# Optimization experiments

Measured on AMD Instinct MI355X. Metric: run time of the kernel, lower is better.

## Reference

```python
import jax, jax.numpy as jnp
import numpy as np

B, D, N_CLASSES = 8192, 128, 50


def setup_inputs() -> dict:
    key = jax.random.key(0)
    k1, k2, k3 = jax.random.split(key, 3)
    anchor = jax.random.normal(k1, (B, D), dtype=jnp.float32)
    target = jax.random.normal(k2, (B, D), dtype=jnp.float32)
    labels = jax.random.randint(k3, (B,), 0, N_CLASSES)
    return {"anchor": anchor, "target": target, "labels": labels}


def reference(anchor, target, labels):
    # Faithful vectorization of QuadrupletLoss.nt_xent_loss.
    # Note: the original hardcodes temperature 0.05 (ignores self.temp).
    TEMP = 0.05
    n = labels.shape[0]
    diff = labels[:, None] != labels[None, :]                      # mask2: [B,B]
    same_off = (labels[:, None] == labels[None, :]) & ~jnp.eye(n, dtype=bool)  # mask

    # d[j, m] = <anchor[j], target[m]> / 0.05
    d = jnp.matmul(anchor, target.T) / TEMP                        # [B,B]
    neg = jnp.where(diff, d, -jnp.inf)
    mx = jax.lax.stop_gradient(jnp.max(neg, axis=1))               # maxdot.detach() per j
    mx = jnp.where(jnp.isfinite(mx), mx, 0.0)
    # s[j] = sum_{m: labels[m]!=labels[j]} exp(d[j,m] - mx[j])  (exp(-inf)=0 masks out)
    s = jnp.sum(jnp.exp(neg - mx[:, None]), axis=1)                # [B]

    # Inner double loop: nds[i] = sum over j with labels[j]!=labels[i] of s[j]
    difff = diff.astype(s.dtype)
    nds = difff @ s                                                # [B]
    negcount = jnp.sum(difff, axis=1)                              # negtivesum

    x = jnp.where(negcount > 0, nds / jnp.where(negcount > 0, negcount, 1.0), nds)
    log_prob = -jnp.log(x + 1e-12)                                 # constant across cols
    mask_sum = jnp.sum(same_off, axis=1)
    # (mask * log_prob).sum(1) / clamp(mask_sum,1) == log_prob where mask_sum>0 else 0
    pos_logits = jnp.where(mask_sum > 0, log_prob, 0.0)
    return -jnp.mean(pos_logits)
```

## Files before the change

### kernel.cpp

```cpp
#include <hip/hip_runtime.h>
#include <float.h>
#include <math.h>

typedef __attribute__((ext_vector_type(8))) short short8;
typedef __attribute__((ext_vector_type(8))) _Float16 half8;
typedef __attribute__((ext_vector_type(4))) float f32x4;

constexpr int B_N  = 8192;
constexpr int D_KK = 128;
constexpr int NCLS = 50;
constexpr int NCHUNK = 8;
constexpr int BLK_ROWS = 64;
constexpr int TCOLS = 64;
constexpr float C_SCALE = 28.853900817779268f;
constexpr float MARGIN  = 40.0f;
constexpr float NEG_LOW  = -1.0e5f;
constexpr float NEG_MASK = -1.0e30f;

__device__ __forceinline__ float exp2fast(float x) { return __builtin_amdgcn_exp2f(x); }

__device__ __forceinline__ void async_copy16(void* lds, const void* g) {
    __builtin_amdgcn_global_load_lds((const __attribute__((address_space(1))) unsigned int*)g,
                                     (__attribute__((address_space(3))) unsigned int*)lds,
                                     16, 0, 0);
}

__global__ void tof16_kernel(const float* __restrict__ a, const float* __restrict__ b,
                             short* __restrict__ aH, short* __restrict__ bH)
{
    const int NPER = B_N * D_KK / 8;
    int i = blockIdx.x * blockDim.x + threadIdx.x;
    const float* src = (i < NPER) ? a : b;
    short*       dst = (i < NPER) ? aH : bH;
    const float  sc  = (i < NPER) ? C_SCALE : 1.0f;
    int j = (i < NPER) ? i : i - NPER;
    const f32x4* sp = (const f32x4*)(src + (size_t)j * 8);
    f32x4 v0 = sp[0], v1 = sp[1];
    short8 h;
#pragma unroll
    for (int e = 0; e < 4; ++e) {
        h[e]     = __builtin_bit_cast(short, (_Float16)(sc * v0[e]));
        h[e + 4] = __builtin_bit_cast(short, (_Float16)(sc * v1[e]));
    }
    *(short8*)(dst + (size_t)j * 8) = h;
}

__global__ __launch_bounds__(256, 4)
void rowstats_kernel(const short* __restrict__ aH, const short* __restrict__ bH,
                     const int* __restrict__ labels,
                     float* __restrict__ pmx, float* __restrict__ ps)
{
    __shared__ __align__(16) char bbuf[2][TCOLS * 256];
    __shared__ float mergebuf[BLK_ROWS][2];

    const int bid   = blockIdx.x;
    const int chunk = bid & (NCHUNK - 1);
    const int R0 = (bid >> 3) * BLK_ROWS;
    const int C0 = chunk * (B_N / NCHUNK);

    const int tid = threadIdx.x;
    const int wid = tid >> 6, l = tid & 63;
    const int l15 = l & 15, l16 = l >> 4;
    const int wr = wid >> 1, wc = wid & 1;

    half8 aF[2][4];
#pragma unroll
    for (int mf = 0; mf < 2; ++mf) {
        const int arow = R0 + wr * 32 + mf * 16 + l15;
#pragma unroll
        for (int ks = 0; ks < 4; ++ks)
            aF[mf][ks] = __builtin_bit_cast(half8,
                *(const short8*)(aH + (size_t)arow * D_KK + ks * 32 + l16 * 8));
    }

    int labA[8];
#pragma unroll
    for (int mf = 0; mf < 2; ++mf)
#pragma unroll
        for (int r = 0; r < 4; ++r)
            labA[mf * 4 + r] = labels[R0 + wr * 32 + mf * 16 + l16 * 4 + r];

    float mx[8], sm[8];
#pragma unroll
    for (int i = 0; i < 8; ++i) { mx[i] = NEG_LOW; sm[i] = 0.0f; }

    const int NT = (B_N / NCHUNK) / TCOLS;

#define STAGE(tile, bsel)                                                            \
    {                                                                                \
        _Pragma("unroll")                                                            \
        for (int q = 0; q < 4; ++q) {                                                \
            int col = q * 16 + (tid >> 4);                                           \
            int gslot = (tid & 15) ^ (col & 7);                                      \
            const short* gp = bH + (size_t)(C0 + (tile) * TCOLS + col) * D_KK + gslot * 8; \
            char* lp = &bbuf[bsel][q * 4096 + tid * 16];                             \
            async_copy16(lp, gp);                                                    \
        }                                                                            \
    }

    STAGE(0, 0);
    __syncthreads();

    for (int t = 0; t < NT; ++t) {
        const int cur = t & 1;
        if (t + 1 < NT) STAGE(t + 1, cur ^ 1);

        f32x4 acc[2][2];
#pragma unroll
        for (int mf = 0; mf < 2; ++mf)
#pragma unroll
            for (int nf = 0; nf < 2; ++nf) acc[mf][nf] = f32x4{0.f, 0.f, 0.f, 0.f};

#pragma unroll
        for (int ks = 0; ks < 4; ++ks) {
            half8 bF[2];
#pragma unroll
            for (int nf = 0; nf < 2; ++nf) {
                int col  = wc * 32 + nf * 16 + l15;
                int slot = (ks * 4 + l16) ^ (col & 7);
                bF[nf] = __builtin_bit_cast(half8,
                    *(const short8*)(&bbuf[cur][col * 256 + slot * 16]));
            }
#pragma unroll
            for (int mf = 0; mf < 2; ++mf)
#pragma unroll
                for (int nf = 0; nf < 2; ++nf)
                    acc[mf][nf] = __builtin_amdgcn_mfma_f32_16x16x32_f16(
                        aF[mf][ks], bF[nf], acc[mf][nf], 0, 0, 0);
        }

        const int colB = C0 + t * TCOLS;
        int lB[2];
#pragma unroll
        for (int nf = 0; nf < 2; ++nf) lB[nf] = labels[colB + wc * 32 + nf * 16 + l15];

#pragma unroll
        for (int mf = 0; mf < 2; ++mf) {
            float gm = fmaxf(fmaxf(fmaxf(acc[mf][0][0], acc[mf][0][1]),
                                   fmaxf(acc[mf][0][2], acc[mf][0][3])),
                             fmaxf(fmaxf(acc[mf][1][0], acc[mf][1][1]),
                                   fmaxf(acc[mf][1][2], acc[mf][1][3])));
            int sk = 1;
#pragma unroll
            for (int r = 0; r < 4; ++r) sk &= (gm < mx[mf * 4 + r] - MARGIN) ? 1 : 0;
            if (!__all(sk)) {
#pragma unroll
                for (int r = 0; r < 4; ++r) {
                    const int i = mf * 4 + r;
                    float v0 = (lB[0] != labA[i]) ? acc[mf][0][r] : NEG_MASK;
                    float v1 = (lB[1] != labA[i]) ? acc[mf][1][r] : NEG_MASK;
                    float nm = fmaxf(mx[i], fmaxf(v0, v1));
                    float e  = exp2fast(v0 - nm) + exp2fast(v1 - nm);
                    sm[i] = sm[i] * exp2fast(mx[i] - nm) + e;
                    mx[i] = nm;
                }
            }
        }
        __syncthreads();
    }

#pragma unroll
    for (int i = 0; i < 8; ++i) {
#pragma unroll
        for (int off = 1; off < 16; off <<= 1) {
            float m2 = __shfl_xor(mx[i], off);
            float s2 = __shfl_xor(sm[i], off);
            float nm = fmaxf(mx[i], m2);
            sm[i] = sm[i] * exp2fast(mx[i] - nm) + s2 * exp2fast(m2 - nm);
            mx[i] = nm;
        }
    }

    if (wc == 1 && l15 == 0) {
#pragma unroll
        for (int mf = 0; mf < 2; ++mf)
#pragma unroll
            for (int r = 0; r < 4; ++r) {
                int rl = wr * 32 + mf * 16 + l16 * 4 + r;
                mergebuf[rl][0] = mx[mf * 4 + r];
                mergebuf[rl][1] = sm[mf * 4 + r];
            }
    }
    __syncthreads();
    if (wc == 0 && l15 == 0) {
#pragma unroll
        for (int mf = 0; mf < 2; ++mf)
#pragma unroll
            for (int r = 0; r < 4; ++r) {
                const int i = mf * 4 + r;
                int rl = wr * 32 + mf * 16 + l16 * 4 + r;
                float m2 = mergebuf[rl][0], s2 = mergebuf[rl][1];
                float nm = fmaxf(mx[i], m2);
                float s  = sm[i] * exp2fast(mx[i] - nm) + s2 * exp2fast(m2 - nm);
                pmx[chunk * B_N + R0 + rl] = nm;
                ps [chunk * B_N + R0 + rl] = s;
            }
    }
#undef STAGE
}

__global__ void classsum_kernel(const float* __restrict__ pmx, const float* __restrict__ ps,
                                const int* __restrict__ labels,
                                float* __restrict__ classSum, unsigned int* __restrict__ classCnt)
{
    __shared__ float        csL[NCLS];
    __shared__ unsigned int ccL[NCLS];
    int t = threadIdx.x;
    if (t < NCLS) { csL[t] = 0.0f; ccL[t] = 0u; }
    __syncthreads();

    int j = blockIdx.x * blockDim.x + t;
    float m = -FLT_MAX, s = 0.0f;
#pragma unroll
    for (int c = 0; c < NCHUNK; ++c) {
        float m2 = pmx[(size_t)c * B_N + j];
        float s2 = ps [(size_t)c * B_N + j];
        float nm = fmaxf(m, m2);
        s = s * exp2fast(m - nm) + s2 * exp2fast(m2 - nm);
        m = nm;
    }
    int lab = labels[j];
    atomicAdd(&csL[lab], s);
    atomicAdd(&ccL[lab], 1u);
    __syncthreads();
    if (t < NCLS) {
        atomicAdd(&classSum[t], csL[t]);
        atomicAdd(&classCnt[t], ccL[t]);
    }
}

__global__ void loss_kernel(const float* __restrict__ classSum,
                            const unsigned int* __restrict__ classCnt,
                            float* __restrict__ out)
{
    int c = threadIdx.x;
    float cs        = (c < NCLS) ? classSum[c] : 0.0f;
    unsigned int cc = (c < NCLS) ? classCnt[c] : 0u;

    float tot = cs;
#pragma unroll
    for (int off = 1; off < 64; off <<= 1) tot += __shfl_xor(tot, off);

    float contrib = 0.0f;
    if (c < NCLS && cc > 0u) {
        float negc = (float)(B_N - (int)cc);
        float nds  = tot - cs;
        float x    = (negc > 0.0f) ? (nds / negc) : nds;
        float lp   = (cc >= 2u) ? (-logf(x + 1e-12f)) : 0.0f;
        contrib = (float)cc * lp;
    }
#pragma unroll
    for (int off = 1; off < 64; off <<= 1) contrib += __shfl_xor(contrib, off);
    if (c == 0) out[0] = -(contrib / (float)B_N);
}

extern "C" void kernel_launch(void* const* d_in, const int* in_sizes, int n_in,
                              void* d_out, int out_size, void* d_ws, size_t ws_size,
                              hipStream_t stream)
{
    const float* anchor = (const float*)d_in[0];
    const float* target = (const float*)d_in[1];
    const int*   labels = (const int*)d_in[2];
    float* out = (float*)d_out;

    const size_t PLANE = (size_t)B_N * D_KK * sizeof(short);
    char* ws = (char*)d_ws;
    short* aH = (short*)(ws + 0 * PLANE);
    short* bH = (short*)(ws + 1 * PLANE);
    float* ps  = (float*)(ws + 2 * PLANE);
    float* pmx = (float*)(ws + 2 * PLANE + sizeof(float) * NCHUNK * B_N);
    char*  cls = ws + 2 * PLANE + 2 * sizeof(float) * NCHUNK * B_N;
    float*        classSum = (float*)cls;
    unsigned int* classCnt = (unsigned int*)(cls + 256);

    hipMemsetAsync(classSum, 0, 512, stream);

    tof16_kernel<<<2 * (B_N * D_KK / 8) / 256, 256, 0, stream>>>(anchor, target, aH, bH);
    rowstats_kernel<<<(B_N / BLK_ROWS) * NCHUNK, 256, 0, stream>>>(aH, bH, labels, pmx, ps);
    classsum_kernel<<<B_N / 256, 256, 0, stream>>>(pmx, ps, labels, classSum, classCnt);
    loss_kernel<<<1, 64, 0, stream>>>(classSum, classCnt, out);
}
```

Before: 57.36 us.

## Drop LDS staging; load B fragments directly from global in k-major layout

```diff
diff --git a/kernel.cpp b/kernel.cpp
--- a/kernel.cpp
+++ b/kernel.cpp
@@ -9,9 +9,8 @@
 constexpr int B_N  = 8192;
 constexpr int D_KK = 128;
 constexpr int NCLS = 50;
-constexpr int NCHUNK = 8;
-constexpr int BLK_ROWS = 64;
-constexpr int TCOLS = 64;
+constexpr int NCHUNK = 16;
+constexpr int CCOLS = B_N / NCHUNK;
 constexpr float C_SCALE = 28.853900817779268f;
 constexpr float MARGIN  = 40.0f;
 constexpr float NEG_LOW  = -1.0e5f;
@@ -19,54 +18,56 @@
 
 __device__ __forceinline__ float exp2fast(float x) { return __builtin_amdgcn_exp2f(x); }
 
-__device__ __forceinline__ void async_copy16(void* lds, const void* g) {
-    __builtin_amdgcn_global_load_lds((const __attribute__((address_space(1))) unsigned int*)g,
-                                     (__attribute__((address_space(3))) unsigned int*)lds,
-                                     16, 0, 0);
-}
-
-__global__ void tof16_kernel(const float* __restrict__ a, const float* __restrict__ b,
-                             short* __restrict__ aH, short* __restrict__ bH)
+__global__ void prep_kernel(const float* __restrict__ a, const float* __restrict__ b,
+                            short* __restrict__ aH, short* __restrict__ bT)
 {
     const int NPER = B_N * D_KK / 8;
     int i = blockIdx.x * blockDim.x + threadIdx.x;
-    const float* src = (i < NPER) ? a : b;
-    short*       dst = (i < NPER) ? aH : bH;
-    const float  sc  = (i < NPER) ? C_SCALE : 1.0f;
-    int j = (i < NPER) ? i : i - NPER;
-    const f32x4* sp = (const f32x4*)(src + (size_t)j * 8);
-    f32x4 v0 = sp[0], v1 = sp[1];
-    short8 h;
-#pragma unroll
-    for (int e = 0; e < 4; ++e) {
-        h[e]     = __builtin_bit_cast(short, (_Float16)(sc * v0[e]));
-        h[e + 4] = __builtin_bit_cast(short, (_Float16)(sc * v1[e]));
-    }
-    *(short8*)(dst + (size_t)j * 8) = h;
+    if (i < NPER) {
+        const f32x4* sp = (const f32x4*)(a + (size_t)i * 8);
+        f32x4 v0 = sp[0], v1 = sp[1];
+        short8 h;
+#pragma unroll
+        for (int e = 0; e < 4; ++e) {
+            h[e]     = __builtin_bit_cast(short, (_Float16)(C_SCALE * v0[e]));
+            h[e + 4] = __builtin_bit_cast(short, (_Float16)(C_SCALE * v1[e]));
+        }
+        *(short8*)(aH + (size_t)i * 8) = h;
+    } else {
+        int j   = i - NPER;
+        int kq  = j & 15;
+        int col = j >> 4;
+        const f32x4* sp = (const f32x4*)(b + (size_t)col * D_KK + kq * 8);
+        f32x4 v0 = sp[0], v1 = sp[1];
+        short8 h;
+#pragma unroll
+        for (int e = 0; e < 4; ++e) {
+            h[e]     = __builtin_bit_cast(short, (_Float16)v0[e]);
+            h[e + 4] = __builtin_bit_cast(short, (_Float16)v1[e]);
+        }
+        *(short8*)(bT + (size_t)kq * B_N * 8 + (size_t)col * 8) = h;
+    }
 }
 
 __global__ __launch_bounds__(256, 4)
-void rowstats_kernel(const short* __restrict__ aH, const short* __restrict__ bH,
+void rowstats_kernel(const short* __restrict__ aH, const short* __restrict__ bT,
                      const int* __restrict__ labels,
                      float* __restrict__ pmx, float* __restrict__ ps)
 {
-    __shared__ __align__(16) char bbuf[2][TCOLS * 256];
-    __shared__ float mergebuf[BLK_ROWS][2];
-
     const int bid   = blockIdx.x;
     const int chunk = bid & (NCHUNK - 1);
-    const int R0 = (bid >> 3) * BLK_ROWS;
-    const int C0 = chunk * (B_N / NCHUNK);
+    const int R0    = (bid >> 4) * 128;
+    const int C0    = chunk * CCOLS;
 
     const int tid = threadIdx.x;
     const int wid = tid >> 6, l = tid & 63;
     const int l15 = l & 15, l16 = l >> 4;
-    const int wr = wid >> 1, wc = wid & 1;
+    const int wrow = R0 + wid * 32;
 
     half8 aF[2][4];
 #pragma unroll
     for (int mf = 0; mf < 2; ++mf) {
-        const int arow = R0 + wr * 32 + mf * 16 + l15;
+        const int arow = wrow + mf * 16 + l15;
 #pragma unroll
         for (int ks = 0; ks < 4; ++ks)
             aF[mf][ks] = __builtin_bit_cast(half8,
@@ -78,32 +79,31 @@
     for (int mf = 0; mf < 2; ++mf)
 #pragma unroll
         for (int r = 0; r < 4; ++r)
-            labA[mf * 4 + r] = labels[R0 + wr * 32 + mf * 16 + l16 * 4 + r];
+            labA[mf * 4 + r] = labels[wrow + mf * 16 + l16 * 4 + r];
 
     float mx[8], sm[8];
 #pragma unroll
     for (int i = 0; i < 8; ++i) { mx[i] = NEG_LOW; sm[i] = 0.0f; }
 
-    const int NT = (B_N / NCHUNK) / TCOLS;
-
-#define STAGE(tile, bsel)                                                            \
-    {                                                                                \
-        _Pragma("unroll")                                                            \
-        for (int q = 0; q < 4; ++q) {                                                \
-            int col = q * 16 + (tid >> 4);                                           \
-            int gslot = (tid & 15) ^ (col & 7);                                      \
-            const short* gp = bH + (size_t)(C0 + (tile) * TCOLS + col) * D_KK + gslot * 8; \
-            char* lp = &bbuf[bsel][q * 4096 + tid * 16];                             \
-            async_copy16(lp, gp);                                                    \
-        }                                                                            \
-    }
-
-    STAGE(0, 0);
-    __syncthreads();
-
+    const short* bBase[2][4];
+#pragma unroll
+    for (int nf = 0; nf < 2; ++nf)
+#pragma unroll
+        for (int ks = 0; ks < 4; ++ks)
+            bBase[nf][ks] = bT + (size_t)(ks * 4 + l16) * B_N * 8
+                               + (size_t)(C0 + nf * 16 + l15) * 8;
+
+    const int NT = CCOLS / 32;
+
+#pragma unroll 2
     for (int t = 0; t < NT; ++t) {
-        const int cur = t & 1;
-        if (t + 1 < NT) STAGE(t + 1, cur ^ 1);
+        half8 bF[2][4];
+#pragma unroll
+        for (int nf = 0; nf < 2; ++nf)
+#pragma unroll
+            for (int ks = 0; ks < 4; ++ks)
+                bF[nf][ks] = __builtin_bit_cast(half8,
+                    *(const short8*)(bBase[nf][ks] + t * 256));
 
         f32x4 acc[2][2];
 #pragma unroll
@@ -112,27 +112,18 @@
             for (int nf = 0; nf < 2; ++nf) acc[mf][nf] = f32x4{0.f, 0.f, 0.f, 0.f};
 
 #pragma unroll
-        for (int ks = 0; ks < 4; ++ks) {
-            half8 bF[2];
-#pragma unroll
-            for (int nf = 0; nf < 2; ++nf) {
-                int col  = wc * 32 + nf * 16 + l15;
-                int slot = (ks * 4 + l16) ^ (col & 7);
-                bF[nf] = __builtin_bit_cast(half8,
-                    *(const short8*)(&bbuf[cur][col * 256 + slot * 16]));
-            }
+        for (int ks = 0; ks < 4; ++ks)
 #pragma unroll
             for (int mf = 0; mf < 2; ++mf)
 #pragma unroll
                 for (int nf = 0; nf < 2; ++nf)
                     acc[mf][nf] = __builtin_amdgcn_mfma_f32_16x16x32_f16(
-                        aF[mf][ks], bF[nf], acc[mf][nf], 0, 0, 0);
-        }
-
-        const int colB = C0 + t * TCOLS;
+                        aF[mf][ks], bF[nf][ks], acc[mf][nf], 0, 0, 0);
+
+        const int colB = C0 + t * 32;
         int lB[2];
 #pragma unroll
-        for (int nf = 0; nf < 2; ++nf) lB[nf] = labels[colB + wc * 32 + nf * 16 + l15];
+        for (int nf = 0; nf < 2; ++nf) lB[nf] = labels[colB + nf * 16 + l15];
 
 #pragma unroll
         for (int mf = 0; mf < 2; ++mf) {
@@ -156,7 +147,6 @@
                 }
             }
         }
-        __syncthreads();
     }
 
 #pragma unroll
@@ -170,33 +160,16 @@
             mx[i] = nm;
         }
     }
-
-    if (wc == 1 && l15 == 0) {
+    if (l15 == 0) {
 #pragma unroll
         for (int mf = 0; mf < 2; ++mf)
 #pragma unroll
             for (int r = 0; r < 4; ++r) {
-                int rl = wr * 32 + mf * 16 + l16 * 4 + r;
-                mergebuf[rl][0] = mx[mf * 4 + r];
-                mergebuf[rl][1] = sm[mf * 4 + r];
+                int row = wrow + mf * 16 + l16 * 4 + r;
+                pmx[chunk * B_N + row] = mx[mf * 4 + r];
+                ps [chunk * B_N + row] = sm[mf * 4 + r];
             }
     }
-    __syncthreads();
-    if (wc == 0 && l15 == 0) {
-#pragma unroll
-        for (int mf = 0; mf < 2; ++mf)
-#pragma unroll
-            for (int r = 0; r < 4; ++r) {
-                const int i = mf * 4 + r;
-                int rl = wr * 32 + mf * 16 + l16 * 4 + r;
-                float m2 = mergebuf[rl][0], s2 = mergebuf[rl][1];
-                float nm = fmaxf(mx[i], m2);
-                float s  = sm[i] * exp2fast(mx[i] - nm) + s2 * exp2fast(m2 - nm);
-                pmx[chunk * B_N + R0 + rl] = nm;
-                ps [chunk * B_N + R0 + rl] = s;
-            }
-    }
-#undef STAGE
 }
 
 __global__ void classsum_kernel(const float* __restrict__ pmx, const float* __restrict__ ps,
@@ -266,7 +239,7 @@
     const size_t PLANE = (size_t)B_N * D_KK * sizeof(short);
     char* ws = (char*)d_ws;
     short* aH = (short*)(ws + 0 * PLANE);
-    short* bH = (short*)(ws + 1 * PLANE);
+    short* bT = (short*)(ws + 1 * PLANE);
     float* ps  = (float*)(ws + 2 * PLANE);
     float* pmx = (float*)(ws + 2 * PLANE + sizeof(float) * NCHUNK * B_N);
     char*  cls = ws + 2 * PLANE + 2 * sizeof(float) * NCHUNK * B_N;
@@ -275,8 +248,8 @@
 
     hipMemsetAsync(classSum, 0, 512, stream);
 
-    tof16_kernel<<<2 * (B_N * D_KK / 8) / 256, 256, 0, stream>>>(anchor, target, aH, bH);
-    rowstats_kernel<<<(B_N / BLK_ROWS) * NCHUNK, 256, 0, stream>>>(aH, bH, labels, pmx, ps);
+    prep_kernel<<<2 * (B_N * D_KK / 8) / 256, 256, 0, stream>>>(anchor, target, aH, bT);
+    rowstats_kernel<<<(B_N / 128) * NCHUNK, 256, 0, stream>>>(aH, bT, labels, pmx, ps);
     classsum_kernel<<<B_N / 256, 256, 0, stream>>>(pmx, ps, labels, classSum, classCnt);
     loss_kernel<<<1, 64, 0, stream>>>(classSum, classCnt, out);
 }
```

After: 55.15 us. 3.9% less time.
